# Kernel optimization log

Hardware: AMD Instinct MI355X
Metric: run time of the kernel (lower is better)

Reference implementation:

```python
import jax, jax.numpy as jnp
import numpy as np

B, N_PER = 1048576, 32
MAX_COUNT = 5  # counts >= 5 lumped into the '>4' bucket (severity 3)


def setup_inputs() -> dict:
    key = jax.random.key(0)
    k1, k2, k3 = jax.random.split(key, 3)
    x1 = jax.random.uniform(k1, (B, N_PER), dtype=jnp.float32)
    x2 = jax.random.uniform(k2, (B, N_PER), dtype=jnp.float32)
    x3 = jax.random.uniform(k3, (B, N_PER), dtype=jnp.float32)
    return {"x1": x1, "x2": x2, "x3": x3}


def _count_distribution(p):
    # p: [B, N] independent fact probabilities.
    # Poisson-binomial DP over facts with count capped at MAX_COUNT (absorbing).
    b = p.shape[0]
    init = jnp.zeros((b, MAX_COUNT + 1), p.dtype).at[:, 0].set(1.0)

    def step(c, pi):
        pi = pi[:, None]                              # [B,1]
        shifted = jnp.pad(c[:, :-1], ((0, 0), (1, 0)))  # count+1
        new = c * (1.0 - pi) + shifted * pi
        # absorbing top bucket: staying in >=MAX_COUNT regardless of pi
        new = new.at[:, -1].add(c[:, -1] * pi[:, 0])
        return new, None

    counts, _ = jax.lax.scan(step, init, p.T)  # scan over facts axis
    return counts  # [B, MAX_COUNT+1]


def reference(x1, x2, x3):
    p = jnp.concatenate([x1, x2, x3], axis=1)  # [B, 96]
    c = _count_distribution(p)
    # severity(0): n==0; severity(1): 1<=n<=2; severity(2): 3<=n<=4;
    # severity(3): n>4; severity(4): never derivable -> 0
    sev = jnp.stack(
        [c[:, 0], c[:, 1] + c[:, 2], c[:, 3] + c[:, 4], c[:, 5],
         jnp.zeros_like(c[:, 0])],
        axis=1,
    )
    return sev  # [B, 5]
```

## Files before the change

### kernel.cpp

```cpp
#include <hip/hip_runtime.h>


#define THREADS 256

__global__ __launch_bounds__(THREADS, 4) void hemorrhage_kernel(
    const float* __restrict__ x1,
    const float* __restrict__ x2,
    const float* __restrict__ x3,
    float* __restrict__ out)
{
    const int row = blockIdx.x * THREADS + threadIdx.x;

    const float4* __restrict__ r1 = (const float4*)(x1 + (size_t)row * 32);
    const float4* __restrict__ r2 = (const float4*)(x2 + (size_t)row * 32);
    const float4* __restrict__ r3 = (const float4*)(x3 + (size_t)row * 32);

    float4 v[24];
#pragma unroll
    for (int j = 0; j < 8; ++j) v[j] = r1[j];
#pragma unroll
    for (int j = 0; j < 8; ++j) v[8 + j] = r2[j];
#pragma unroll
    for (int j = 0; j < 8; ++j) v[16 + j] = r3[j];

    float a0 = 1.0f, a1 = 0.0f, a2 = 0.0f, a3 = 0.0f, a4 = 0.0f;

#define STEP(P)                              \
    do {                                     \
        const float p_ = (P);                \
        a4 = fmaf(p_, a3 - a4, a4);          \
        a3 = fmaf(p_, a2 - a3, a3);          \
        a2 = fmaf(p_, a1 - a2, a2);          \
        a1 = fmaf(p_, a0 - a1, a1);          \
        a0 = fmaf(-p_, a0, a0);              \
    } while (0)

#pragma unroll
    for (int j = 0; j < 24; ++j) {
        STEP(v[j].x);
        STEP(v[j].y);
        STEP(v[j].z);
        STEP(v[j].w);
    }
#undef STEP

    const float c5 = 1.0f - (((a0 + a1) + (a2 + a3)) + a4);

    float* __restrict__ o = out + (size_t)row * 5;
    o[0] = a0;
    o[1] = a1 + a2;
    o[2] = a3 + a4;
    o[3] = c5;
    o[4] = 0.0f;
}

extern "C" void kernel_launch(void* const* d_in, const int* in_sizes, int n_in,
                              void* d_out, int out_size, void* d_ws, size_t ws_size,
                              hipStream_t stream) {
    const float* x1 = (const float*)d_in[0];
    const float* x2 = (const float*)d_in[1];
    const float* x3 = (const float*)d_in[2];
    float* out = (float*)d_out;

    const int rows = in_sizes[0] / 32;
    const int blocks = rows / THREADS;
    hemorrhage_kernel<<<blocks, THREADS, 0, stream>>>(x1, x2, x3, out);
}
```

Baseline: 362.4 us.

## Coalesce global loads and transpose rows through padded shared memory

Threads in a block now load contiguous float4 chunks of each input so that global reads are coalesced. The data is then scattered into a padded LDS tile (stride 33) so each thread can read its own row for the sequential DP. The three inputs are processed in phases, with the next input's loads overlapping the current compute. This adds LDS traffic and several block-wide barriers, and halves the threads per block.

```diff
diff --git a/kernel.cpp b/kernel.cpp
--- a/kernel.cpp
+++ b/kernel.cpp
@@ -1,7 +1,9 @@
 #include <hip/hip_runtime.h>
 
 
-#define THREADS 256
+#define THREADS 128
+#define ROWS_PER_BLOCK 128
+#define STRIDE 33
 
 __global__ __launch_bounds__(THREADS, 4) void hemorrhage_kernel(
     const float* __restrict__ x1,
@@ -9,21 +11,31 @@
     const float* __restrict__ x3,
     float* __restrict__ out)
 {
-    const int row = blockIdx.x * THREADS + threadIdx.x;
+    __shared__ float lds[ROWS_PER_BLOCK * STRIDE];
 
-    const float4* __restrict__ r1 = (const float4*)(x1 + (size_t)row * 32);
-    const float4* __restrict__ r2 = (const float4*)(x2 + (size_t)row * 32);
-    const float4* __restrict__ r3 = (const float4*)(x3 + (size_t)row * 32);
+    const int t = threadIdx.x;
+    const size_t blockBase = (size_t)blockIdx.x * ROWS_PER_BLOCK * 32;
 
-    float4 v[24];
+    const float4* __restrict__ g1 = (const float4*)(x1 + blockBase);
+    const float4* __restrict__ g2 = (const float4*)(x2 + blockBase);
+    const float4* __restrict__ g3 = (const float4*)(x3 + blockBase);
+
+    float4 v[8], w[8];
 #pragma unroll
-    for (int j = 0; j < 8; ++j) v[j] = r1[j];
+    for (int j = 0; j < 8; ++j) v[j] = g1[t + THREADS * j];
 #pragma unroll
-    for (int j = 0; j < 8; ++j) v[8 + j] = r2[j];
-#pragma unroll
-    for (int j = 0; j < 8; ++j) v[16 + j] = r3[j];
+    for (int j = 0; j < 8; ++j) w[j] = g2[t + THREADS * j];
 
     float a0 = 1.0f, a1 = 0.0f, a2 = 0.0f, a3 = 0.0f, a4 = 0.0f;
+
+#define WRITE_LDS(SRC)                                        \
+    _Pragma("unroll")                                         \
+    for (int j = 0; j < 8; ++j) {                             \
+        const int f_ = t + THREADS * j;                       \
+        float* wp_ = &lds[(f_ >> 3) * STRIDE + (f_ & 7) * 4]; \
+        wp_[0] = (SRC)[j].x; wp_[1] = (SRC)[j].y;             \
+        wp_[2] = (SRC)[j].z; wp_[3] = (SRC)[j].w;             \
+    }
 
 #define STEP(P)                              \
     do {                                     \
@@ -35,18 +47,33 @@
         a0 = fmaf(-p_, a0, a0);              \
     } while (0)
 
+#define COMPUTE32()                                           \
+    _Pragma("unroll")                                         \
+    for (int k = 0; k < 32; ++k) STEP(lds[t * STRIDE + k]);
+
+    WRITE_LDS(v);
+    __syncthreads();
 #pragma unroll
-    for (int j = 0; j < 24; ++j) {
-        STEP(v[j].x);
-        STEP(v[j].y);
-        STEP(v[j].z);
-        STEP(v[j].w);
-    }
+    for (int j = 0; j < 8; ++j) v[j] = g3[t + THREADS * j];
+    COMPUTE32();
+    __syncthreads();
+
+    WRITE_LDS(w);
+    __syncthreads();
+    COMPUTE32();
+    __syncthreads();
+
+    WRITE_LDS(v);
+    __syncthreads();
+    COMPUTE32();
+
+#undef COMPUTE32
 #undef STEP
+#undef WRITE_LDS
 
     const float c5 = 1.0f - (((a0 + a1) + (a2 + a3)) + a4);
 
-    float* __restrict__ o = out + (size_t)row * 5;
+    float* __restrict__ o = out + (size_t)(blockIdx.x * ROWS_PER_BLOCK + t) * 5;
     o[0] = a0;
     o[1] = a1 + a2;
     o[2] = a3 + a4;
@@ -63,6 +90,6 @@
     float* out = (float*)d_out;
 
     const int rows = in_sizes[0] / 32;
-    const int blocks = rows / THREADS;
+    const int blocks = rows / ROWS_PER_BLOCK;
     hemorrhage_kernel<<<blocks, THREADS, 0, stream>>>(x1, x2, x3, out);
 }
```

Result: faster. 354.7 us (-2.1%).

## Split each row across 8 lanes with shuffle-based polynomial merge and prefetching grid-stride loop

Applied to the files above, without the earlier changes.

Each row is now handled by 8 lanes that each run the capped DP over 12 probabilities loaded as coalesced float4s. The partial count distributions are then combined by truncated polynomial multiplication through xor shuffles. A persistent grid-stride loop prefetches the next group's loads before computing the current one, and the stores are spread across lanes. The aim is fully coalesced, bandwidth-bound loads instead of each thread reading 384 contiguous bytes. The cost is extra shuffle and multiply work, plus hardcoded group and grid constants tied to the input size.

```diff
diff --git a/kernel.cpp b/kernel.cpp
--- a/kernel.cpp
+++ b/kernel.cpp
@@ -2,28 +2,29 @@
 
 
 #define THREADS 256
+#define NGROUPS 32768
+#define GRID    2048
 
-__global__ __launch_bounds__(THREADS, 4) void hemorrhage_kernel(
+__global__ __launch_bounds__(THREADS, 8) void hemorrhage_kernel(
     const float* __restrict__ x1,
     const float* __restrict__ x2,
     const float* __restrict__ x3,
     float* __restrict__ out)
 {
-    const int row = blockIdx.x * THREADS + threadIdx.x;
+    const int t = threadIdx.x;
+    const int m = t & 7;
+    const int stride = gridDim.x;
 
-    const float4* __restrict__ r1 = (const float4*)(x1 + (size_t)row * 32);
-    const float4* __restrict__ r2 = (const float4*)(x2 + (size_t)row * 32);
-    const float4* __restrict__ r3 = (const float4*)(x3 + (size_t)row * 32);
+    const float4* __restrict__ f1 = (const float4*)x1;
+    const float4* __restrict__ f2 = (const float4*)x2;
+    const float4* __restrict__ f3 = (const float4*)x3;
 
-    float4 v[24];
-#pragma unroll
-    for (int j = 0; j < 8; ++j) v[j] = r1[j];
-#pragma unroll
-    for (int j = 0; j < 8; ++j) v[8 + j] = r2[j];
-#pragma unroll
-    for (int j = 0; j < 8; ++j) v[16 + j] = r3[j];
+    int g = blockIdx.x;
 
-    float a0 = 1.0f, a1 = 0.0f, a2 = 0.0f, a3 = 0.0f, a4 = 0.0f;
+    unsigned idx = (unsigned)g * 256u + (unsigned)t;
+    float4 c1 = f1[idx];
+    float4 c2 = f2[idx];
+    float4 c3 = f3[idx];
 
 #define STEP(P)                              \
     do {                                     \
@@ -35,23 +36,68 @@
         a0 = fmaf(-p_, a0, a0);              \
     } while (0)
 
+    for (;;) {
+        const int gn = g + stride;
+        const bool have_next = (gn < NGROUPS);
+        float4 n1, n2, n3;
+        if (have_next) {
+            const unsigned nidx = (unsigned)gn * 256u + (unsigned)t;
+            n1 = f1[nidx];
+            n2 = f2[nidx];
+            n3 = f3[nidx];
+        }
+
+        float a0 = 1.0f, a1 = 0.0f, a2 = 0.0f, a3 = 0.0f, a4 = 0.0f;
+        STEP(c1.x); STEP(c1.y); STEP(c1.z); STEP(c1.w);
+        STEP(c2.x); STEP(c2.y); STEP(c2.z); STEP(c2.w);
+        STEP(c3.x); STEP(c3.y); STEP(c3.z); STEP(c3.w);
+
 #pragma unroll
-    for (int j = 0; j < 24; ++j) {
-        STEP(v[j].x);
-        STEP(v[j].y);
-        STEP(v[j].z);
-        STEP(v[j].w);
+        for (int d = 1; d < 8; d <<= 1) {
+            const float b0 = __shfl_xor(a0, d);
+            const float b1 = __shfl_xor(a1, d);
+            const float b2 = __shfl_xor(a2, d);
+            const float b3 = __shfl_xor(a3, d);
+            const float b4 = __shfl_xor(a4, d);
+
+            float n0v = a0 * b0;
+            float n1v = a0 * b1;
+            n1v = fmaf(a1, b0, n1v);
+            float n2v = a0 * b2;
+            n2v = fmaf(a1, b1, n2v);
+            n2v = fmaf(a2, b0, n2v);
+            float n3v = a0 * b3;
+            n3v = fmaf(a1, b2, n3v);
+            n3v = fmaf(a2, b1, n3v);
+            n3v = fmaf(a3, b0, n3v);
+            float n4v = a0 * b4;
+            n4v = fmaf(a1, b3, n4v);
+            n4v = fmaf(a2, b2, n4v);
+            n4v = fmaf(a3, b1, n4v);
+            n4v = fmaf(a4, b0, n4v);
+
+            a0 = n0v; a1 = n1v; a2 = n2v; a3 = n3v; a4 = n4v;
+        }
+
+        if (m < 5) {
+            const float c5 = 1.0f - (((a0 + a1) + (a2 + a3)) + a4);
+            float v;
+            switch (m) {
+                case 0: v = a0; break;
+                case 1: v = a1 + a2; break;
+                case 2: v = a3 + a4; break;
+                case 3: v = c5; break;
+                default: v = 0.0f; break;
+            }
+            const size_t row = (size_t)g * 32 + (t >> 3);
+            out[row * 5 + m] = v;
+        }
+
+        if (!have_next) break;
+        c1 = n1; c2 = n2; c3 = n3;
+        g = gn;
     }
 #undef STEP
-
-    const float c5 = 1.0f - (((a0 + a1) + (a2 + a3)) + a4);
-
-    float* __restrict__ o = out + (size_t)row * 5;
-    o[0] = a0;
-    o[1] = a1 + a2;
-    o[2] = a3 + a4;
-    o[3] = c5;
-    o[4] = 0.0f;
 }
 
 extern "C" void kernel_launch(void* const* d_in, const int* in_sizes, int n_in,
@@ -62,7 +108,5 @@
     const float* x3 = (const float*)d_in[2];
     float* out = (float*)d_out;
 
-    const int rows = in_sizes[0] / 32;
-    const int blocks = rows / THREADS;
-    hemorrhage_kernel<<<blocks, THREADS, 0, stream>>>(x1, x2, x3, out);
+    hemorrhage_kernel<<<GRID, THREADS, 0, stream>>>(x1, x2, x3, out);
 }
```

New measurement: 357.6 us. About the same (-1.3%).
